# Kernel optimization log

Hardware: AMD Instinct MI355X
Metric: run time of the kernel (lower is better)

The kernel has to match this reference:

```python
import jax, jax.numpy as jnp
import numpy as np

EPS = 1e-5


def _conv(x, k, pad):
    # x: (B,C,H,W), k: (Co,Ci,kh,kw)
    return jax.lax.conv_general_dilated(
        x, k, window_strides=(1, 1), padding=pad,
        dimension_numbers=("NCHW", "OIHW", "NCHW"))


def _prop_rows(x, k, b, g, bt, m, v, a, reverse):
    # direction 'D' (reverse=False) or 'U' (reverse=True).
    # conv on a 1xW stripe with 3x3 pad1 only uses the middle kernel row.
    kmid = k[:, :, 1:2, :]  # (C,C,1,3)
    # conv(current + res) = (K*current + b) + K*res ; precompute per-row part.
    pre = _conv(x, kmid, [(0, 0), (1, 1)]) + b[None, :, None, None]  # (B,C,H,W)
    inv = g / jnp.sqrt(v + EPS)
    mn, bn_b = m[None, :, None], bt[None, :, None]
    inv3 = inv[None, :, None]

    def step(res, pre_i):  # res, pre_i: (B,C,W)
        h = pre_i + _conv(res[:, :, None, :], kmid, [(0, 0), (1, 1)])[:, :, 0, :]
        y = (h - mn) * inv3 + bn_b
        y = jnp.where(y >= 0, y, a * y)  # PReLU (single shared param)
        return y, y

    B, _, H, W = x.shape
    res0 = jnp.zeros((B, k.shape[0], W), x.dtype)
    xs = jnp.moveaxis(pre, 2, 0)  # (H,B,C,W)
    _, ys = jax.lax.scan(step, res0, xs, reverse=reverse)
    return jnp.moveaxis(ys, 0, 2)  # (B,C,H,W)


def _prop_cols(x, k, b, g, bt, m, v, a, reverse):
    # direction 'R' (reverse=False) or 'L' (reverse=True); only middle kernel col used.
    kmid = k[:, :, :, 1:2]  # (C,C,3,1)
    pre = _conv(x, kmid, [(1, 1), (0, 0)]) + b[None, :, None, None]  # (B,C,H,W)
    inv = g / jnp.sqrt(v + EPS)
    mn, bn_b = m[None, :, None], bt[None, :, None]
    inv3 = inv[None, :, None]

    def step(res, pre_i):  # res, pre_i: (B,C,H)
        h = pre_i + _conv(res[:, :, :, None], kmid, [(1, 1), (0, 0)])[:, :, :, 0]
        y = (h - mn) * inv3 + bn_b
        y = jnp.where(y >= 0, y, a * y)
        return y, y

    B, _, H, W = x.shape
    res0 = jnp.zeros((B, k.shape[0], H), x.dtype)
    xs = jnp.moveaxis(pre, 3, 0)  # (W,B,C,H)
    _, ys = jax.lax.scan(step, res0, xs, reverse=reverse)
    return jnp.moveaxis(ys, 0, 3)  # (B,C,H,W)


def setup_inputs() -> dict:
    key = jax.random.key(0)
    ks = jax.random.split(key, 16)
    B, C, H, W = 8, 128, 160, 160
    x = jax.random.normal(ks[0], (B, C, H, W), jnp.float32)
    # std ~ 1/sqrt(fan_in=C*3) keeps the recurrence stable
    kernels = jax.random.normal(ks[1], (4, C, C, 3, 3), jnp.float32) * 0.04
    biases = jax.random.normal(ks[2], (4, C), jnp.float32) * 0.05
    bn_gamma = 1.0 + 0.1 * jax.random.normal(ks[3], (4, C), jnp.float32)
    bn_beta = 0.1 * jax.random.normal(ks[4], (4, C), jnp.float32)
    bn_mean = 0.1 * jax.random.normal(ks[5], (4, C), jnp.float32)
    bn_var = 1.0 + 0.1 * jax.random.uniform(ks[6], (4, C), jnp.float32)
    prelu_a = jnp.full((4,), 0.25, jnp.float32)
    fus_w = jax.random.normal(ks[7], (C, 4 * C), jnp.float32) * 0.04
    fus_b = jax.random.normal(ks[8], (C,), jnp.float32) * 0.05
    fbn_gamma = 1.0 + 0.1 * jax.random.normal(ks[9], (C,), jnp.float32)
    fbn_beta = 0.1 * jax.random.normal(ks[10], (C,), jnp.float32)
    fbn_mean = 0.1 * jax.random.normal(ks[11], (C,), jnp.float32)
    fbn_var = 1.0 + 0.1 * jax.random.uniform(ks[12], (C,), jnp.float32)
    return dict(x=x, kernels=kernels, biases=biases, bn_gamma=bn_gamma,
                bn_beta=bn_beta, bn_mean=bn_mean, bn_var=bn_var,
                prelu_a=prelu_a, fus_w=fus_w, fus_b=fus_b,
                fbn_gamma=fbn_gamma, fbn_beta=fbn_beta, fbn_mean=fbn_mean,
                fbn_var=fbn_var)


def reference(x, kernels, biases, bn_gamma, bn_beta, bn_mean, bn_var, prelu_a,
              fus_w, fus_b, fbn_gamma, fbn_beta, fbn_mean, fbn_var):
    def p(i):
        return (kernels[i], biases[i], bn_gamma[i], bn_beta[i], bn_mean[i],
                bn_var[i], prelu_a[i])

    feat_D = _prop_rows(x, *p(0), reverse=False)
    feat_U = _prop_rows(x, *p(1), reverse=True)
    feat_R = _prop_cols(x, *p(2), reverse=False)
    feat_L = _prop_cols(x, *p(3), reverse=True)
    feat = jnp.concatenate([feat_D, feat_U, feat_R, feat_L], axis=1)  # (B,4C,H,W)
    out = jnp.einsum("oc,bchw->bohw", fus_w, feat) + fus_b[None, :, None, None]
    inv = fbn_gamma / jnp.sqrt(fbn_var + EPS)
    out = (out - fbn_mean[None, :, None, None]) * inv[None, :, None, None] \
        + fbn_beta[None, :, None, None]
    return jax.nn.relu(out)
```

## Files before the change

### kernel.cpp

```cpp
#include <hip/hip_runtime.h>
#include <stdint.h>


typedef __attribute__((ext_vector_type(8))) __bf16 bf16x8;
typedef __attribute__((ext_vector_type(4))) float f32x4;

#define DEV static __device__ __forceinline__

DEV unsigned short f2bf(float f) {
  union { float f; unsigned int u; } v; v.f = f;
  unsigned int u = v.u;
  u += 0x7fffu + ((u >> 16) & 1u);
  return (unsigned short)(u >> 16);
}
DEV float bf2f(unsigned short s) {
  union { float f; unsigned int u; } v; v.u = ((unsigned int)s) << 16;
  return v.f;
}
DEV f32x4 mfma16(bf16x8 a, bf16x8 b, f32x4 c) {
  return __builtin_amdgcn_mfma_f32_16x16x32_bf16(a, b, c, 0, 0, 0);
}
DEV void barrier_lds() {
  asm volatile("s_waitcnt lgkmcnt(0)\n\ts_barrier" ::: "memory");
}

constexpr int Hc = 160, Wc = 160, Bn = 8, Cc = 128;
constexpr int CHUNK = 32, NCH = 5;
constexpr int SPAD = 136;

constexpr long WS_XT    = 0;
constexpr long WS_WPREP = 104857600;
constexpr long WS_EPI   = 105250816;
constexpr long WS_FWT   = 105254912;
constexpr long WS_FEPI  = 105385984;
constexpr long WS_FEAT  = 105387008;
constexpr long WS_EX    = 315102208;
constexpr long WS_TOTAL = 315429888;

__global__ void prep_kernel(const float* __restrict__ kern, const float* __restrict__ bias,
                            const float* __restrict__ bg, const float* __restrict__ bb,
                            const float* __restrict__ bm, const float* __restrict__ bv,
                            const float* __restrict__ fw, const float* __restrict__ fb2,
                            const float* __restrict__ fg, const float* __restrict__ fbt,
                            const float* __restrict__ fm, const float* __restrict__ fv,
                            unsigned short* __restrict__ wprep, float2* __restrict__ epi,
                            unsigned short* __restrict__ fwT, float2* __restrict__ fepi)
{
  int idx = blockIdx.x * 256 + threadIdx.x;
  if (idx < 196608) {
    int c = idx & 127;
    int t = (idx >> 7) % 3;
    int o = (idx / 384) & 127;
    int d = idx / 49152;
    int kh = (d < 2) ? 1 : t;
    int kw = (d < 2) ? t : 1;
    wprep[idx] = f2bf(kern[(((d * 128 + o) * 128 + c) * 3 + kh) * 3 + kw]);
  }
  int i2 = idx - 196608;
  if (i2 >= 0 && i2 < 65536) fwT[i2] = f2bf(fw[i2]);
  int i3 = idx - 262144;
  if (i3 >= 0 && i3 < 512) {
    float sc = bg[i3] / sqrtf(bv[i3] + 1e-5f);
    epi[i3] = make_float2(sc, (bias[i3] - bm[i3]) * sc + bb[i3]);
  }
  int i4 = idx - 262656;
  if (i4 >= 0 && i4 < 128) {
    float sc = fg[i4] / sqrtf(fv[i4] + 1e-5f);
    fepi[i4] = make_float2(sc, (fb2[i4] - fm[i4]) * sc + fbt[i4]);
  }
}

__global__ void transpose_kernel(const float* __restrict__ x, float* __restrict__ xT)
{
  __shared__ float tile[32][33];
  int b = blockIdx.z, h = blockIdx.y;
  int c0 = (blockIdx.x / 5) * 32, w0 = (blockIdx.x % 5) * 32;
  int tx = threadIdx.x & 31, ty = threadIdx.x >> 5;
#pragma unroll
  for (int r = 0; r < 4; r++) {
    int c = c0 + ty + 8 * r;
    tile[ty + 8 * r][tx] = x[(((long)b * 128 + c) * 160 + h) * 160 + w0 + tx];
  }
  __syncthreads();
#pragma unroll
  for (int r = 0; r < 4; r++) {
    int w = w0 + ty + 8 * r;
    xT[(((long)b * 160 + h) * 160 + w) * 128 + c0 + tx] = tile[tx][ty + 8 * r];
  }
}

__global__ __launch_bounds__(256, 1) void scan_kernel(
    const float* __restrict__ xT, const unsigned short* __restrict__ wprep,
    const float2* __restrict__ epi, const float* __restrict__ prelu_a,
    unsigned short* __restrict__ featbuf, unsigned int* __restrict__ ex)
{
  __shared__ unsigned short sbuf[2][34 * SPAD];

  const int bid = blockIdx.x;
  const int q = bid >> 5;
  const int g = bid & 31;
  const int d = g >> 3, b = g & 7;
  const bool row_mode = (d < 2);
  const bool rev = (d & 1);
  const int u0 = q * CHUNK;
  const int tid = threadIdx.x;
  const int lane = tid & 63;
  const int wv = tid >> 6;
  const int ncol = lane & 15;
  const int kq = lane >> 4;

  const long si = row_mode ? (long)Wc * Cc : (long)Cc;
  const long su = row_mode ? (long)Cc : (long)Wc * Cc;
  const long fi = row_mode ? (long)Wc * 512 : (long)512;
  const long fu = row_mode ? (long)512 : (long)Wc * 512;
  const float* xb = xT + (long)b * Hc * Wc * Cc;
  unsigned short* fbp = featbuf + (long)b * Hc * Wc * 512 + d * 128;

  bf16x8 Bfrag[2][12];
  float2 ep[2];
#pragma unroll
  for (int j = 0; j < 2; j++) {
    const int o = (wv * 2 + j) * 16 + ncol;
    const unsigned short* wp = wprep + ((long)(d * 128 + o)) * 384;
#pragma unroll
    for (int kt = 0; kt < 12; kt++)
      Bfrag[j][kt] = *(const bf16x8*)(wp + kt * 32 + kq * 8);
    ep[j] = epi[d * 128 + o];
  }
  const float aslope = prelu_a[d];

  unsigned int* ex_self = ex + (long)bid * 512;
  const unsigned int* ex_leftp  = ex + (long)(bid - 32) * 512 + 256;
  const unsigned int* ex_rightp = ex + (long)(bid + 32) * 512;

  const int colbase0 = (wv * 2) * 16 + ncol;
  const int colbase1 = (wv * 2 + 1) * 16 + ncol;

  const int oh = tid & 127;
  const bool left_side = (tid < 128);
  const int srow = left_side ? 0 : 33;
  const bool interior = left_side ? (q > 0) : (q < NCH - 1);
  const int ug = left_side ? (u0 - 1) : (u0 + CHUNK);
  const bool ug_ok = (ug >= 0 && ug < 160);

  const int i0 = rev ? (Hc - 1) : 0;
  for (int e = tid; e < 34 * 64; e += 256) {
    const int u = e >> 6, cp = e & 63;
    const int uu = u0 + u - 1;
    unsigned int sv = 0;
    if (uu >= 0 && uu < 160) {
      const float2 xv2 = *(const float2*)(xb + (long)i0 * si + (long)uu * su + cp * 2);
      sv = (unsigned int)f2bf(xv2.x) | ((unsigned int)f2bf(xv2.y) << 16);
    }
    *(unsigned int*)&sbuf[0][u * SPAD + cp * 2] = sv;
  }
  barrier_lds();

#pragma unroll 1
  for (int t = 0; t < 160; t++) {
    const int i = rev ? (159 - t) : t;
    const int inext = rev ? (i - 1) : (i + 1);
    const bool last = (t == 159);
    const int par = t & 1;
    unsigned short* cur = sbuf[t & 1];
    unsigned short* nxt = sbuf[(t & 1) ^ 1];

    float xn[2][2][4];
    float xh = 0.f;
    if (!last) {
      const float* xrow = xb + (long)inext * si;
#pragma unroll
      for (int mt = 0; mt < 2; mt++)
#pragma unroll
        for (int j = 0; j < 2; j++) {
          const int col = j ? colbase1 : colbase0;
#pragma unroll
          for (int r = 0; r < 4; r++) {
            const int row = mt * 16 + kq * 4 + r;
            xn[mt][j][r] = xrow[(long)(u0 + row) * su + col];
          }
        }
      if (ug_ok) xh = xrow[(long)ug * su + oh];
    }

    f32x4 acc[2][2];
#pragma unroll
    for (int mt = 0; mt < 2; mt++)
#pragma unroll
      for (int j = 0; j < 2; j++)
        acc[mt][j] = (f32x4){0.f, 0.f, 0.f, 0.f};
#pragma unroll
    for (int kt = 0; kt < 12; kt++) {
      const int tt = kt >> 2;
      const int c0 = ((kt & 3) << 5) + (kq << 3);
      const bf16x8 A0 = *(const bf16x8*)&cur[(ncol + tt) * SPAD + c0];
      const bf16x8 A1 = *(const bf16x8*)&cur[(16 + ncol + tt) * SPAD + c0];
      acc[0][0] = mfma16(A0, Bfrag[0][kt], acc[0][0]);
      acc[0][1] = mfma16(A0, Bfrag[1][kt], acc[0][1]);
      acc[1][0] = mfma16(A1, Bfrag[0][kt], acc[1][0]);
      acc[1][1] = mfma16(A1, Bfrag[1][kt], acc[1][1]);
    }

    float yf[2][2][4];
    unsigned short yb[2][2][4];
#pragma unroll
    for (int mt = 0; mt < 2; mt++)
#pragma unroll
      for (int j = 0; j < 2; j++)
#pragma unroll
        for (int r = 0; r < 4; r++) {
          float v = acc[mt][j][r] * ep[j].x + ep[j].y;
          v = (v >= 0.f) ? v : (aslope * v);
          yf[mt][j][r] = v;
          yb[mt][j][r] = f2bf(v);
        }

    {
      const unsigned int tagv = ((unsigned int)(t + 1)) << 16;
      if (kq == 0) {
        __hip_atomic_store(&ex_self[par * 128 + colbase0], tagv | (unsigned int)yb[0][0][0],
                           __ATOMIC_RELAXED, __HIP_MEMORY_SCOPE_AGENT);
        __hip_atomic_store(&ex_self[par * 128 + colbase1], tagv | (unsigned int)yb[0][1][0],
                           __ATOMIC_RELAXED, __HIP_MEMORY_SCOPE_AGENT);
      }
      if (kq == 3) {
        __hip_atomic_store(&ex_self[256 + par * 128 + colbase0], tagv | (unsigned int)yb[1][0][3],
                           __ATOMIC_RELAXED, __HIP_MEMORY_SCOPE_AGENT);
        __hip_atomic_store(&ex_self[256 + par * 128 + colbase1], tagv | (unsigned int)yb[1][1][3],
                           __ATOMIC_RELAXED, __HIP_MEMORY_SCOPE_AGENT);
      }
    }

    unsigned short* frow = fbp + (long)i * fi;
#pragma unroll
    for (int mt = 0; mt < 2; mt++)
#pragma unroll
      for (int j = 0; j < 2; j++) {
        const int col = j ? colbase1 : colbase0;
#pragma unroll
        for (int r = 0; r < 4; r++) {
          const int row = mt * 16 + kq * 4 + r;
          frow[(long)(u0 + row) * fu + col] = yb[mt][j][r];
          if (!last)
            nxt[(1 + row) * SPAD + col] = f2bf(xn[mt][j][r] + yf[mt][j][r]);
        }
      }

    if (!last) {
      float yv = 0.f;
      if (interior) {
        const unsigned int* slot = (left_side ? ex_leftp : ex_rightp) + par * 128 + oh;
        unsigned int v = __hip_atomic_load(slot, __ATOMIC_RELAXED, __HIP_MEMORY_SCOPE_AGENT);
        while ((v >> 16) != (unsigned int)(t + 1)) {
          __builtin_amdgcn_s_sleep(1);
          v = __hip_atomic_load(slot, __ATOMIC_RELAXED, __HIP_MEMORY_SCOPE_AGENT);
        }
        yv = bf2f((unsigned short)(v & 0xffff));
      }
      unsigned short sv = 0;
      if (ug_ok) sv = f2bf(xh + yv);
      nxt[srow * SPAD + oh] = sv;
    }
    barrier_lds();
  }
}

__global__ __launch_bounds__(256, 1) void fusion_kernel(
    const unsigned short* __restrict__ featbuf, const unsigned short* __restrict__ fwT,
    const float2* __restrict__ fepi, float* __restrict__ out)
{
  __shared__ unsigned short At[32 * 520];
  const int bx = blockIdx.x;
  const int b = bx / 800, mb = bx - b * 800;
  const long m0 = (long)mb * 32;
  const int tid = threadIdx.x, lane = tid & 63, wv = tid >> 6;
  const int ncol = lane & 15, kq = lane >> 4;

  const unsigned short* fp = featbuf + ((long)b * 25600 + m0) * 512;
#pragma unroll
  for (int rr = 0; rr < 8; rr++) {
    const int e = tid + rr * 256;
    const int m = e >> 6, kp = e & 63;
    *(bf16x8*)&At[m * 520 + kp * 8] = *(const bf16x8*)(fp + (long)m * 512 + kp * 8);
  }
  bf16x8 Bf[2][16];
  float2 fe[2];
#pragma unroll
  for (int j = 0; j < 2; j++) {
    const int o = (wv * 2 + j) * 16 + ncol;
    const unsigned short* wp = fwT + (long)o * 512;
#pragma unroll
    for (int kt = 0; kt < 16; kt++)
      Bf[j][kt] = *(const bf16x8*)(wp + kt * 32 + kq * 8);
    fe[j] = fepi[o];
  }
  __syncthreads();

  f32x4 acc[2][2];
#pragma unroll
  for (int mt = 0; mt < 2; mt++)
#pragma unroll
    for (int j = 0; j < 2; j++)
      acc[mt][j] = (f32x4){0.f, 0.f, 0.f, 0.f};
#pragma unroll
  for (int kt = 0; kt < 16; kt++) {
    const bf16x8 A0 = *(const bf16x8*)&At[ncol * 520 + kt * 32 + kq * 8];
    const bf16x8 A1 = *(const bf16x8*)&At[(16 + ncol) * 520 + kt * 32 + kq * 8];
    acc[0][0] = mfma16(A0, Bf[0][kt], acc[0][0]);
    acc[0][1] = mfma16(A0, Bf[1][kt], acc[0][1]);
    acc[1][0] = mfma16(A1, Bf[0][kt], acc[1][0]);
    acc[1][1] = mfma16(A1, Bf[1][kt], acc[1][1]);
  }
#pragma unroll
  for (int mt = 0; mt < 2; mt++)
#pragma unroll
    for (int j = 0; j < 2; j++) {
      const int o = (wv * 2 + j) * 16 + ncol;
      const long hw = m0 + mt * 16 + kq * 4;
      f32x4 v;
#pragma unroll
      for (int r = 0; r < 4; r++) {
        const float z = acc[mt][j][r] * fe[j].x + fe[j].y;
        v[r] = (z > 0.f) ? z : 0.f;
      }
      *(f32x4*)(out + ((long)(b * 128 + o)) * 25600 + hw) = v;
    }
}

extern "C" void kernel_launch(void* const* d_in, const int* in_sizes, int n_in,
                              void* d_out, int out_size, void* d_ws, size_t ws_size,
                              hipStream_t stream)
{
  if (ws_size < (size_t)WS_TOTAL) return;

  const float* x        = (const float*)d_in[0];
  const float* kernels  = (const float*)d_in[1];
  const float* biases   = (const float*)d_in[2];
  const float* bn_gamma = (const float*)d_in[3];
  const float* bn_beta  = (const float*)d_in[4];
  const float* bn_mean  = (const float*)d_in[5];
  const float* bn_var   = (const float*)d_in[6];
  const float* prelu_a  = (const float*)d_in[7];
  const float* fus_w    = (const float*)d_in[8];
  const float* fus_b    = (const float*)d_in[9];
  const float* fbn_g    = (const float*)d_in[10];
  const float* fbn_b    = (const float*)d_in[11];
  const float* fbn_m    = (const float*)d_in[12];
  const float* fbn_v    = (const float*)d_in[13];

  char* ws = (char*)d_ws;
  float*          xT      = (float*)(ws + WS_XT);
  unsigned short* wprep   = (unsigned short*)(ws + WS_WPREP);
  float2*         epi     = (float2*)(ws + WS_EPI);
  unsigned short* fwT     = (unsigned short*)(ws + WS_FWT);
  float2*         fepi    = (float2*)(ws + WS_FEPI);
  unsigned short* featbuf = (unsigned short*)(ws + WS_FEAT);
  unsigned int*   ex      = (unsigned int*)(ws + WS_EX);
  float*          out     = (float*)d_out;

  prep_kernel<<<1027, 256, 0, stream>>>(kernels, biases, bn_gamma, bn_beta, bn_mean, bn_var,
                                        fus_w, fus_b, fbn_g, fbn_b, fbn_m, fbn_v,
                                        wprep, epi, fwT, fepi);
  transpose_kernel<<<dim3(20, 160, 8), 256, 0, stream>>>(x, xT);
  scan_kernel<<<160, 256, 0, stream>>>(xT, wprep, epi, prelu_a, featbuf, ex);
  fusion_kernel<<<6400, 256, 0, stream>>>(featbuf, fwT, fepi, out);
}
```

Baseline: 681.6 us.

## Split scan into 16-row chunks, pair opposite directions per 512-thread block

The recurrent scan kernel now cuts each sequence into 10 chunks of 16 instead of 5 chunks of 32. Each 512-thread block runs both opposite directions (D/U or R/L) for one batch and chunk, with one half of the block per direction. This halves the serial MFMA and epilogue work per wave per step and spreads the scan over more wavefronts. In exchange there are twice as many chunk boundaries, so more cross-block halo exchange and spin-waits. Per-thread global offsets are also precomputed outside the time loop.

```diff
diff --git a/kernel.cpp b/kernel.cpp
--- a/kernel.cpp
+++ b/kernel.cpp
@@ -24,8 +24,9 @@
   asm volatile("s_waitcnt lgkmcnt(0)\n\ts_barrier" ::: "memory");
 }
 
-constexpr int Hc = 160, Wc = 160, Bn = 8, Cc = 128;
-constexpr int CHUNK = 32, NCH = 5;
+constexpr int Hc = 160, Wc = 160, Cc = 128;
+constexpr int CHUNK = 16, NCH = 10;
+constexpr int ROWS = 18;
 constexpr int SPAD = 136;
 
 constexpr long WS_XT    = 0;
@@ -35,7 +36,7 @@
 constexpr long WS_FEPI  = 105385984;
 constexpr long WS_FEAT  = 105387008;
 constexpr long WS_EX    = 315102208;
-constexpr long WS_TOTAL = 315429888;
+constexpr long WS_TOTAL = 315757568;
 
 __global__ void prep_kernel(const float* __restrict__ kern, const float* __restrict__ bias,
                             const float* __restrict__ bg, const float* __restrict__ bb,
@@ -89,38 +90,43 @@
   }
 }
 
-__global__ __launch_bounds__(256, 1) void scan_kernel(
+__global__ __launch_bounds__(512, 2) void scan_kernel(
     const float* __restrict__ xT, const unsigned short* __restrict__ wprep,
     const float2* __restrict__ epi, const float* __restrict__ prelu_a,
     unsigned short* __restrict__ featbuf, unsigned int* __restrict__ ex)
 {
-  __shared__ unsigned short sbuf[2][34 * SPAD];
+  __shared__ unsigned short sbuf[2][2][ROWS * SPAD];
 
   const int bid = blockIdx.x;
-  const int q = bid >> 5;
-  const int g = bid & 31;
-  const int d = g >> 3, b = g & 7;
-  const bool row_mode = (d < 2);
-  const bool rev = (d & 1);
-  const int u0 = q * CHUNK;
+  const int q = bid >> 4;
+  const int g = bid & 15;
+  const int p = g >> 3, b = g & 7;
   const int tid = threadIdx.x;
+  const int wv = tid >> 6;
+  const int s = wv >> 2;
+  const int wl = wv & 3;
   const int lane = tid & 63;
-  const int wv = tid >> 6;
   const int ncol = lane & 15;
   const int kq = lane >> 4;
-
+  const int d = p * 2 + s;
+  const bool rev = (s != 0);
+  const int u0 = q * CHUNK;
+
+  const bool row_mode = (p == 0);
   const long si = row_mode ? (long)Wc * Cc : (long)Cc;
-  const long su = row_mode ? (long)Cc : (long)Wc * Cc;
+  const int  su = row_mode ? Cc : Wc * Cc;
   const long fi = row_mode ? (long)Wc * 512 : (long)512;
-  const long fu = row_mode ? (long)512 : (long)Wc * 512;
+  const int  fu = row_mode ? 512 : Wc * 512;
   const float* xb = xT + (long)b * Hc * Wc * Cc;
   unsigned short* fbp = featbuf + (long)b * Hc * Wc * 512 + d * 128;
 
   bf16x8 Bfrag[2][12];
   float2 ep[2];
+  int colj[2];
 #pragma unroll
   for (int j = 0; j < 2; j++) {
-    const int o = (wv * 2 + j) * 16 + ncol;
+    const int o = (wl * 2 + j) * 16 + ncol;
+    colj[j] = o;
     const unsigned short* wp = wprep + ((long)(d * 128 + o)) * 384;
 #pragma unroll
     for (int kt = 0; kt < 12; kt++)
@@ -129,22 +135,32 @@
   }
   const float aslope = prelu_a[d];
 
-  unsigned int* ex_self = ex + (long)bid * 512;
-  const unsigned int* ex_leftp  = ex + (long)(bid - 32) * 512 + 256;
-  const unsigned int* ex_rightp = ex + (long)(bid + 32) * 512;
-
-  const int colbase0 = (wv * 2) * 16 + ncol;
-  const int colbase1 = (wv * 2 + 1) * 16 + ncol;
-
+  int xoff[2][4], foff[2][4];
+#pragma unroll
+  for (int j = 0; j < 2; j++)
+#pragma unroll
+    for (int r = 0; r < 4; r++) {
+      const int row = kq * 4 + r;
+      xoff[j][r] = (u0 + row) * su + colj[j];
+      foff[j][r] = (u0 + row) * fu + colj[j];
+    }
+
+  const int sid = d * 80 + b * 10 + q;
+  unsigned int* ex_self = ex + (long)sid * 512;
+
+  const int hside = (tid >> 7) & 1;
   const int oh = tid & 127;
-  const bool left_side = (tid < 128);
-  const int srow = left_side ? 0 : 33;
-  const bool interior = left_side ? (q > 0) : (q < NCH - 1);
-  const int ug = left_side ? (u0 - 1) : (u0 + CHUNK);
+  const bool interior = hside ? (q < NCH - 1) : (q > 0);
+  const int ug = hside ? (u0 + CHUNK) : (u0 - 1);
   const bool ug_ok = (ug >= 0 && ug < 160);
+  const int srow = hside ? (ROWS - 1) : 0;
+  const int xhoff = ug_ok ? (ug * su + oh) : 0;
+  const unsigned int* ex_nbr = hside ? (ex + (long)(sid + 1) * 512)
+                                     : (ex + (long)(sid - 1) * 512 + 256);
 
   const int i0 = rev ? (Hc - 1) : 0;
-  for (int e = tid; e < 34 * 64; e += 256) {
+  const int tids = tid & 255;
+  for (int e = tids; e < ROWS * 64; e += 256) {
     const int u = e >> 6, cp = e & 63;
     const int uu = u0 + u - 1;
     unsigned int sv = 0;
@@ -152,7 +168,7 @@
       const float2 xv2 = *(const float2*)(xb + (long)i0 * si + (long)uu * su + cp * 2);
       sv = (unsigned int)f2bf(xv2.x) | ((unsigned int)f2bf(xv2.y) << 16);
     }
-    *(unsigned int*)&sbuf[0][u * SPAD + cp * 2] = sv;
+    *(unsigned int*)&sbuf[s][0][u * SPAD + cp * 2] = sv;
   }
   barrier_lds();
 
@@ -162,94 +178,75 @@
     const int inext = rev ? (i - 1) : (i + 1);
     const bool last = (t == 159);
     const int par = t & 1;
-    unsigned short* cur = sbuf[t & 1];
-    unsigned short* nxt = sbuf[(t & 1) ^ 1];
-
-    float xn[2][2][4];
+    const unsigned short* cur = sbuf[s][par];
+    unsigned short* nxt = sbuf[s][par ^ 1];
+
+    const float* xrow = xb + (long)inext * si;
+    float xn[2][4];
     float xh = 0.f;
     if (!last) {
-      const float* xrow = xb + (long)inext * si;
-#pragma unroll
-      for (int mt = 0; mt < 2; mt++)
-#pragma unroll
-        for (int j = 0; j < 2; j++) {
-          const int col = j ? colbase1 : colbase0;
-#pragma unroll
-          for (int r = 0; r < 4; r++) {
-            const int row = mt * 16 + kq * 4 + r;
-            xn[mt][j][r] = xrow[(long)(u0 + row) * su + col];
-          }
-        }
-      if (ug_ok) xh = xrow[(long)ug * su + oh];
-    }
-
-    f32x4 acc[2][2];
-#pragma unroll
-    for (int mt = 0; mt < 2; mt++)
 #pragma unroll
       for (int j = 0; j < 2; j++)
-        acc[mt][j] = (f32x4){0.f, 0.f, 0.f, 0.f};
+#pragma unroll
+        for (int r = 0; r < 4; r++)
+          xn[j][r] = xrow[xoff[j][r]];
+      if (ug_ok) xh = xrow[xhoff];
+    }
+
+    f32x4 acc[2];
+    acc[0] = (f32x4){0.f, 0.f, 0.f, 0.f};
+    acc[1] = (f32x4){0.f, 0.f, 0.f, 0.f};
 #pragma unroll
     for (int kt = 0; kt < 12; kt++) {
       const int tt = kt >> 2;
       const int c0 = ((kt & 3) << 5) + (kq << 3);
       const bf16x8 A0 = *(const bf16x8*)&cur[(ncol + tt) * SPAD + c0];
-      const bf16x8 A1 = *(const bf16x8*)&cur[(16 + ncol + tt) * SPAD + c0];
-      acc[0][0] = mfma16(A0, Bfrag[0][kt], acc[0][0]);
-      acc[0][1] = mfma16(A0, Bfrag[1][kt], acc[0][1]);
-      acc[1][0] = mfma16(A1, Bfrag[0][kt], acc[1][0]);
-      acc[1][1] = mfma16(A1, Bfrag[1][kt], acc[1][1]);
-    }
-
-    float yf[2][2][4];
-    unsigned short yb[2][2][4];
-#pragma unroll
-    for (int mt = 0; mt < 2; mt++)
-#pragma unroll
-      for (int j = 0; j < 2; j++)
-#pragma unroll
-        for (int r = 0; r < 4; r++) {
-          float v = acc[mt][j][r] * ep[j].x + ep[j].y;
-          v = (v >= 0.f) ? v : (aslope * v);
-          yf[mt][j][r] = v;
-          yb[mt][j][r] = f2bf(v);
-        }
+      acc[0] = mfma16(A0, Bfrag[0][kt], acc[0]);
+      acc[1] = mfma16(A0, Bfrag[1][kt], acc[1]);
+    }
+
+    float yf[2][4];
+    unsigned short yb[2][4];
+#pragma unroll
+    for (int j = 0; j < 2; j++)
+#pragma unroll
+      for (int r = 0; r < 4; r++) {
+        float v = acc[j][r] * ep[j].x + ep[j].y;
+        v = (v >= 0.f) ? v : (aslope * v);
+        yf[j][r] = v;
+        yb[j][r] = f2bf(v);
+      }
 
     {
       const unsigned int tagv = ((unsigned int)(t + 1)) << 16;
       if (kq == 0) {
-        __hip_atomic_store(&ex_self[par * 128 + colbase0], tagv | (unsigned int)yb[0][0][0],
+        __hip_atomic_store(&ex_self[par * 128 + colj[0]], tagv | (unsigned int)yb[0][0],
                            __ATOMIC_RELAXED, __HIP_MEMORY_SCOPE_AGENT);
-        __hip_atomic_store(&ex_self[par * 128 + colbase1], tagv | (unsigned int)yb[0][1][0],
+        __hip_atomic_store(&ex_self[par * 128 + colj[1]], tagv | (unsigned int)yb[1][0],
                            __ATOMIC_RELAXED, __HIP_MEMORY_SCOPE_AGENT);
       }
       if (kq == 3) {
-        __hip_atomic_store(&ex_self[256 + par * 128 + colbase0], tagv | (unsigned int)yb[1][0][3],
+        __hip_atomic_store(&ex_self[256 + par * 128 + colj[0]], tagv | (unsigned int)yb[0][3],
                            __ATOMIC_RELAXED, __HIP_MEMORY_SCOPE_AGENT);
-        __hip_atomic_store(&ex_self[256 + par * 128 + colbase1], tagv | (unsigned int)yb[1][1][3],
+        __hip_atomic_store(&ex_self[256 + par * 128 + colj[1]], tagv | (unsigned int)yb[1][3],
                            __ATOMIC_RELAXED, __HIP_MEMORY_SCOPE_AGENT);
       }
     }
 
     unsigned short* frow = fbp + (long)i * fi;
 #pragma unroll
-    for (int mt = 0; mt < 2; mt++)
-#pragma unroll
-      for (int j = 0; j < 2; j++) {
-        const int col = j ? colbase1 : colbase0;
-#pragma unroll
-        for (int r = 0; r < 4; r++) {
-          const int row = mt * 16 + kq * 4 + r;
-          frow[(long)(u0 + row) * fu + col] = yb[mt][j][r];
-          if (!last)
-            nxt[(1 + row) * SPAD + col] = f2bf(xn[mt][j][r] + yf[mt][j][r]);
-        }
+    for (int j = 0; j < 2; j++)
+#pragma unroll
+      for (int r = 0; r < 4; r++) {
+        frow[foff[j][r]] = yb[j][r];
+        if (!last)
+          nxt[(1 + kq * 4 + r) * SPAD + colj[j]] = f2bf(xn[j][r] + yf[j][r]);
       }
 
     if (!last) {
       float yv = 0.f;
       if (interior) {
-        const unsigned int* slot = (left_side ? ex_leftp : ex_rightp) + par * 128 + oh;
+        const unsigned int* slot = ex_nbr + par * 128 + oh;
         unsigned int v = __hip_atomic_load(slot, __ATOMIC_RELAXED, __HIP_MEMORY_SCOPE_AGENT);
         while ((v >> 16) != (unsigned int)(t + 1)) {
           __builtin_amdgcn_s_sleep(1);
@@ -362,6 +359,6 @@
                                         fus_w, fus_b, fbn_g, fbn_b, fbn_m, fbn_v,
                                         wprep, epi, fwT, fepi);
   transpose_kernel<<<dim3(20, 160, 8), 256, 0, stream>>>(x, xT);
-  scan_kernel<<<160, 256, 0, stream>>>(xT, wprep, epi, prelu_a, featbuf, ex);
+  scan_kernel<<<160, 512, 0, stream>>>(xT, wprep, epi, prelu_a, featbuf, ex);
   fusion_kernel<<<6400, 256, 0, stream>>>(featbuf, fwT, fepi, out);
 }
```

Measured after the change: 609.3 us. -10.6%, faster.
